# Kernel tuning notes

Hardware: AMD Instinct MI355X
Metric: run time of the kernel (lower is better)

The kernel has to match this reference:

```python
import jax, jax.numpy as jnp
import numpy as np
from jax import lax

DN = ('NCHW', 'OIHW', 'NCHW')


def setup_inputs() -> dict:
    key = jax.random.key(0)
    ks = jax.random.split(key, 7)
    B, IC, OC, H, W = 8, 64, 64, 128, 128
    return {
        'x': jax.random.normal(ks[0], (B, IC, H, W), jnp.float32),
        'w3': jax.random.normal(ks[1], (OC, IC, 3, 3), jnp.float32) * 0.05,
        'b3': jax.random.normal(ks[2], (OC,), jnp.float32) * 0.05,
        'w5': jax.random.normal(ks[3], (OC, IC, 5, 5), jnp.float32) * 0.05,
        'b5': jax.random.normal(ks[4], (OC,), jnp.float32) * 0.05,
        'wr': jax.random.normal(ks[5], (OC, 10, 1, 1), jnp.float32) * 0.1,
        'br': jax.random.normal(ks[6], (OC,), jnp.float32) * 0.05,
    }


def reference(x, w3, b3, w5, b5, wr, br):
    # Two 'same' convs (k=3 pad 1, k=5 pad 2) as in layers['5']
    y3 = lax.conv_general_dilated(x, w3, (1, 1), 'SAME', dimension_numbers=DN) + b3[None, :, None, None]
    y5 = lax.conv_general_dilated(x, w5, (1, 1), 'SAME', dimension_numbers=DN) + b5[None, :, None, None]
    B, C, H, W = y3.shape
    # The nested pad/crop loop == 9 zero-padded unit shifts of y3:
    # stackedFeatures order per channel: [y5, shift(sh=0,sw=0..2), shift(sh=1,...), ...]
    # shifted[h, w] = y3[h + 1 - sw, w + 1 - sh] with zero padding.
    P = jnp.pad(y3, ((0, 0), (0, 0), (1, 1), (1, 1)))
    shifts = [P[:, :, 2 - sw:2 - sw + H, 2 - sh:2 - sh + W]
              for sh in range(3) for sw in range(3)]
    stacked = jnp.stack([y5] + shifts, axis=2)  # [B, C, 10, H, W]
    # remap: grouped 1x1 conv, groups=OC, 10 in-channels per group
    out = jnp.einsum('bcghw,cg->bchw', stacked, wr[:, :, 0, 0]) + br[None, :, None, None]
    return out
```

## Files before the change

### kernel.cpp

```cpp
#include <hip/hip_runtime.h>

typedef unsigned short u16;
typedef unsigned int u32;
typedef __attribute__((ext_vector_type(8))) short short8;
typedef __attribute__((ext_vector_type(4))) short short4v;
typedef __attribute__((ext_vector_type(4))) float floatx4;

#define XP 72

__device__ __forceinline__ float bf2f(u16 u) {
    u32 b = ((u32)u) << 16;
    return __builtin_bit_cast(float, b);
}
__device__ __forceinline__ u16 f2bf(float f) {
    u32 b = __builtin_bit_cast(u32, f);
    b += 0x7FFFu + ((b >> 16) & 1u);
    return (u16)(b >> 16);
}

typedef __attribute__((address_space(3))) u16 lds_u16;
typedef const __attribute__((address_space(1))) u16 glob_u16;
__device__ __forceinline__ void gl_lds16(const u16* g, u16* l) {
    __builtin_amdgcn_global_load_lds((glob_u16*)g, (lds_u16*)l, 16, 0, 0);
}

__device__ __forceinline__ float load_any(const void* p, int i, int isf32) {
    return isf32 ? ((const float*)p)[i] : bf2f(((const u16*)p)[i]);
}

__device__ __forceinline__ int sniff_f(const void* x) {
    u16 u = ((const u16*)x)[2 * (int)threadIdx.x];
    int e = (u >> 7) & 0xFF;
    unsigned long long m = __ballot(e >= 140);
    return __popcll(m) >= 2 ? 1 : 0;
}

#define W5C_BYTE 0
#define SCAL_BYTE 204800
#define V_BYTE 207616
#define FR_BYTE 1272576
#define XT_BYTE 2321152
#define N_W5C 102400
#define N_SCAL 704
#define PACK_N2 (N_W5C + N_SCAL)

#define PACK_BLKS ((PACK_N2 + 255) / 256)
#define TRANS_BLKS 4096

__global__ __launch_bounds__(256) void pack_trans(
        const void* __restrict__ x, const void* __restrict__ w3,
        const void* __restrict__ b3, const void* __restrict__ w5,
        const void* __restrict__ b5, const void* __restrict__ wr,
        const void* __restrict__ br,
        u16* __restrict__ w5c, float* __restrict__ scal,
        u16* __restrict__ xt) {
    __shared__ u16 tbuf[32 * XP];
    const int bid = blockIdx.x;
    const int tid = threadIdx.x;
    const int f = sniff_f(x);

    if (bid < PACK_BLKS) {
        const int i = bid * 256 + tid;
        if (i >= PACK_N2) return;
        if (i < N_W5C) {
            int j = i & 7, lane = (i >> 3) & 63, mt = (i >> 9) & 3, ks = i >> 11;
            int oc = mt * 16 + (lane & 15);
            int k = ks * 32 + ((lane >> 4) & 3) * 8 + j;
            int tap = k >> 6, ic = k & 63;
            int kh = tap / 5, kw = tap - kh * 5;
            int dh = kh - 2, dw = kw - 2;
            float v = load_any(wr, oc * 10, f) * load_any(w5, (oc * 64 + ic) * 25 + tap, f);
            for (int sw = 0; sw < 3; ++sw) {
                int r = dh + sw;
                if (r < 0 || r > 2) continue;
                for (int sh = 0; sh < 3; ++sh) {
                    int c = dw + sh;
                    if (c < 0 || c > 2) continue;
                    v += load_any(wr, oc * 10 + 1 + sh * 3 + sw, f) *
                         load_any(w3, (oc * 64 + ic) * 9 + r * 3 + c, f);
                }
            }
            w5c[i] = f2bf(v);
        } else {
            int i2 = i - N_W5C;
            float v;
            if (i2 < 64) {
                int oc = i2;
                float swr = 0.f;
                for (int g = 1; g <= 9; ++g) swr += load_any(wr, oc * 10 + g, f);
                v = load_any(wr, oc * 10, f) * load_any(b5, oc, f) +
                    swr * load_any(b3, oc, f) + load_any(br, oc, f);
            } else {
                v = load_any(wr, i2 - 64, f);
            }
            scal[i2] = v;
        }
        return;
    }

    {
        const int t2 = bid - PACK_BLKS;
        const int b = t2 >> 9, h = (t2 >> 2) & 127, w0 = (t2 & 3) * 32;
        const int t = tid;
        if (f) {
            const int w2 = t & 15, ic = t >> 4;
#pragma unroll
            for (int p = 0; p < 4; ++p) {
                int icc = ic + p * 16;
                const float* src = (const float*)x +
                    (((size_t)(b * 64 + icc) * 128 + h) * 128 + w0 + 2 * w2);
                float2 v = *(const float2*)src;
                tbuf[(2 * w2) * XP + icc]     = f2bf(v.x);
                tbuf[(2 * w2 + 1) * XP + icc] = f2bf(v.y);
            }
        } else {
            const int w4 = t & 7, ic = t >> 3;
#pragma unroll
            for (int p = 0; p < 2; ++p) {
                int icc = ic + p * 32;
                const u16* src = (const u16*)x +
                    (((size_t)(b * 64 + icc) * 128 + h) * 128 + w0 + 4 * w4);
                short4v v = *(const short4v*)src;
#pragma unroll
                for (int e = 0; e < 4; ++e)
                    tbuf[(4 * w4 + e) * XP + icc] = (u16)v[e];
            }
        }
        __syncthreads();
        const int w = t >> 3, qq = t & 7;
        short8 v = *(const short8*)&tbuf[w * XP + qq * 8];
        *(short8*)(xt + ((size_t)((b * 128 + h) * 128) + w0 + w) * 64 + qq * 8) = v;
    }
}

__global__ __launch_bounds__(256) void virt_y3_mfma(
        const void* __restrict__ x,
        const u16* __restrict__ xt, const void* __restrict__ w3,
        const void* __restrict__ b3, float* __restrict__ V) {
    __shared__ __align__(16) u16 xrow[132 * XP];
    const int side = blockIdx.x, b = blockIdx.y;
    const int tid = threadIdx.x;
    const int f = sniff_f(x);
    const int fixed = (side & 1) ? 127 : 0;
    {
        const int q8 = tid & 7, p0 = tid >> 3;
#pragma unroll
        for (int it = 0; it < 5; ++it) {
            int p = p0 + it * 32;
            if (p < 132) {
                int cc = p - 2;
                short8 v = {0, 0, 0, 0, 0, 0, 0, 0};
                if ((unsigned)cc < 128u) {
                    size_t idx = (side < 2)
                        ? ((size_t)(b * 128 + fixed) * 128 + cc)
                        : ((size_t)(b * 128 + cc) * 128 + fixed);
                    v = *(const short8*)(xt + idx * 64 + q8 * 8);
                }
                *(short8*)&xrow[p * XP + q8 * 8] = v;
            }
        }
    }
    const int wv = tid >> 6, lane = tid & 63, cb = lane & 15, q = lane >> 4;
    const int oc = wv * 16 + cb;
    short8 aaA[6];
#pragma unroll
    for (int ks = 0; ks < 6; ++ks) {
        const int kbase = ks * 32 + q * 8;
        const int kk = kbase >> 6, ic0 = kbase & 63;
        int r, c;
        if (side == 0)      { r = 2;  c = kk; }
        else if (side == 1) { r = 0;  c = kk; }
        else if (side == 2) { r = kk; c = 2;  }
        else                { r = kk; c = 0;  }
        short8 a;
#pragma unroll
        for (int j = 0; j < 8; ++j)
            a[j] = (short)f2bf(load_any(w3, (oc * 64 + ic0 + j) * 9 + r * 3 + c, f));
        aaA[ks] = a;
    }
    __syncthreads();

    floatx4 acc[9];
#pragma unroll
    for (int nt = 0; nt < 9; ++nt) acc[nt] = (floatx4){0.f, 0.f, 0.f, 0.f};
#pragma unroll
    for (int ks = 0; ks < 6; ++ks) {
        const int kbase = ks * 32 + q * 8;
        const int kk = kbase >> 6, ic0 = kbase & 63;
#pragma unroll
        for (int nt = 0; nt < 9; ++nt) {
            int p = nt * 16 + cb + kk;
            if (nt == 8 && p > 131) p = 131;
            short8 bb = *(const short8*)&xrow[p * XP + ic0];
            acc[nt] = __builtin_amdgcn_mfma_f32_16x16x32_bf16(aaA[ks], bb,
                                                              acc[nt], 0, 0, 0);
        }
    }
#pragma unroll
    for (int nt = 0; nt < 9; ++nt) {
        int pos = nt * 16 + cb;
        if (pos < 130) {
#pragma unroll
            for (int reg = 0; reg < 4; ++reg) {
                int oco = wv * 16 + q * 4 + reg;
                V[((size_t)(b * 4 + side) * 130 + pos) * 64 + oco] =
                    acc[nt][reg] + load_any(b3, oco, f);
            }
        }
    }
}

__global__ __launch_bounds__(256) void ring_fix(
        const float* __restrict__ V, const float* __restrict__ scal,
        float* __restrict__ Fr) {
    const int side = blockIdx.x, b = blockIdx.y;
    const float* wrf = scal + 64;
    const float* Vb = V + (size_t)b * 4 * 130 * 64;
    for (int k = 0; k < 8; ++k) {
        const int idx = (blockIdx.z * 8 + k) * 256 + threadIdx.x;
        const int pos = idx >> 6, oc = idx & 63;
        int h, w;
        if (side == 0)      { h = 0;   w = pos; }
        else if (side == 1) { h = 127; w = pos; }
        else if (side == 2) { w = 0;   h = pos; }
        else                { w = 127; h = pos; }
        float s = 0.f;
#pragma unroll
        for (int sh = 0; sh < 3; ++sh)
#pragma unroll
            for (int sw = 0; sw < 3; ++sw) {
                const int qh = h + 1 - sw, qw = w + 1 - sh;
                int sd, pp;
                if (qh == -1)       { sd = 0; pp = qw + 1; }
                else if (qh == 128) { sd = 1; pp = qw + 1; }
                else if (qw == -1)  { sd = 2; pp = qh + 1; }
                else if (qw == 128) { sd = 3; pp = qh + 1; }
                else continue;
                s -= wrf[oc * 10 + 1 + sh * 3 + sw] *
                     Vb[((size_t)sd * 130 + pp) * 64 + oc];
            }
        Fr[((size_t)(b * 4 + side) * 128 + pos) * 64 + oc] = s;
    }
}

__global__ __launch_bounds__(256, 3) void conv_main(
        const void* __restrict__ x,
        const u16* __restrict__ xt, const u16* __restrict__ w5c,
        const float* __restrict__ scal, const float* __restrict__ Fr,
        void* __restrict__ out) {
    __shared__ __align__(16) u16 xs[240 * XP];
    __shared__ __align__(16) u16 wbuf[2][2][2048];
    const int b = blockIdx.z, h0 = blockIdx.y * 8, w0 = blockIdx.x * 16;
    const int tid = threadIdx.x;
    const int wv = tid >> 6, lane = tid & 63;
    const int f = sniff_f(x);

    {
        const int q8 = tid & 7, p0 = tid >> 3;
#pragma unroll
        for (int it = 0; it < 8; ++it) {
            int px = p0 + it * 32;
            if (px < 240) {
                int r = px / 20, c = px - r * 20;
                int gh = h0 + r - 2, gw = w0 + c - 2;
                short8 v = {0, 0, 0, 0, 0, 0, 0, 0};
                if ((unsigned)gh < 128u && (unsigned)gw < 128u)
                    v = *(const short8*)(xt +
                            ((size_t)((b * 128 + gh) * 128 + gw)) * 64 + q8 * 8);
                *(short8*)&xs[px * XP + q8 * 8] = v;
            }
        }
    }
    gl_lds16(w5c + 0 * 2048 + wv * 512 + lane * 8, &wbuf[0][0][wv * 512]);
    gl_lds16(w5c + 1 * 2048 + wv * 512 + lane * 8, &wbuf[0][1][wv * 512]);
    __syncthreads();

    const int cb = lane & 15, q = lane >> 4, wv2 = wv * 2;
    floatx4 acc[4][2];
#pragma unroll
    for (int mt = 0; mt < 4; ++mt)
#pragma unroll
        for (int nt = 0; nt < 2; ++nt)
            acc[mt][nt] = (floatx4){0.f, 0.f, 0.f, 0.f};

#pragma unroll 1
    for (int tap = 0; tap < 25; ++tap) {
        const int p = tap & 1;
        if (tap + 1 < 25) {
            gl_lds16(w5c + (size_t)((tap + 1) * 2 + 0) * 2048 + wv * 512 + lane * 8,
                     &wbuf[p ^ 1][0][wv * 512]);
            gl_lds16(w5c + (size_t)((tap + 1) * 2 + 1) * 2048 + wv * 512 + lane * 8,
                     &wbuf[p ^ 1][1][wv * 512]);
        }
        const int kh = tap / 5, kw = tap - kh * 5;
#pragma unroll
        for (int s = 0; s < 2; ++s) {
            short8 aa[4], bb[2];
#pragma unroll
            for (int mt = 0; mt < 4; ++mt)
                aa[mt] = *(const short8*)&wbuf[p][s][mt * 512 + lane * 8];
#pragma unroll
            for (int nt = 0; nt < 2; ++nt)
                bb[nt] = *(const short8*)&xs[((wv2 + nt + kh) * 20 + cb + kw) * XP +
                                             s * 32 + q * 8];
#pragma unroll
            for (int nt = 0; nt < 2; ++nt)
#pragma unroll
                for (int mt = 0; mt < 4; ++mt)
                    acc[mt][nt] = __builtin_amdgcn_mfma_f32_16x16x32_bf16(
                        aa[mt], bb[nt], acc[mt][nt], 0, 0, 0);
        }
        __syncthreads();
    }

    const float* biasC = scal;
    const float* Frb = Fr + (size_t)b * 4 * 128 * 64;
#pragma unroll
    for (int mt = 0; mt < 4; ++mt)
#pragma unroll
        for (int nt = 0; nt < 2; ++nt) {
            const int gh = h0 + wv2 + nt;
            const int gw = w0 + cb;
            const int oc0 = mt * 16 + q * 4;
            floatx4 s;
#pragma unroll
            for (int reg = 0; reg < 4; ++reg)
                s[reg] = acc[mt][nt][reg] + biasC[oc0 + reg];
            {
                int sd = -1, pp = 0;
                if (gh == 0)        { sd = 0; pp = gw; }
                else if (gh == 127) { sd = 1; pp = gw; }
                else if (gw == 0)   { sd = 2; pp = gh; }
                else if (gw == 127) { sd = 3; pp = gh; }
                if (sd >= 0) {
                    floatx4 fv = *(const floatx4*)(Frb +
                        ((size_t)sd * 128 + pp) * 64 + oc0);
#pragma unroll
                    for (int reg = 0; reg < 4; ++reg) s[reg] += fv[reg];
                }
            }
#pragma unroll
            for (int reg = 0; reg < 4; ++reg) {
                size_t oidx = ((size_t)(b * 64 + oc0 + reg) * 128 + gh) * 128 + gw;
                if (f) ((float*)out)[oidx] = s[reg];
                else   ((u16*)out)[oidx]   = f2bf(s[reg]);
            }
        }
}

extern "C" void kernel_launch(void* const* d_in, const int* in_sizes, int n_in,
                              void* d_out, int out_size, void* d_ws, size_t ws_size,
                              hipStream_t stream) {
    const void* x  = d_in[0];
    const void* w3 = d_in[1];
    const void* b3 = d_in[2];
    const void* w5 = d_in[3];
    const void* b5 = d_in[4];
    const void* wr = d_in[5];
    const void* br = d_in[6];

    u16*   w5c  = (u16*)((char*)d_ws + W5C_BYTE);
    float* scal = (float*)((char*)d_ws + SCAL_BYTE);
    float* V    = (float*)((char*)d_ws + V_BYTE);
    float* Fr   = (float*)((char*)d_ws + FR_BYTE);
    u16*   xt   = (u16*)((char*)d_ws + XT_BYTE);

    pack_trans<<<PACK_BLKS + TRANS_BLKS, 256, 0, stream>>>(
        x, w3, b3, w5, b5, wr, br, w5c, scal, xt);
    virt_y3_mfma<<<dim3(4, 8), 256, 0, stream>>>(x, xt, w3, b3, V);
    ring_fix<<<dim3(4, 8, 4), 256, 0, stream>>>(V, scal, Fr);
    conv_main<<<dim3(8, 16, 8), 256, 0, stream>>>(x, xt, w5c, scal, Fr, d_out);
}
```

Baseline: 167.5 us.

## Double conv_main tile height and stream weights through registers instead of LDS

conv_main's tile grows from 8 to 16 rows, giving 4 rows per wave and a 4x4 MFMA accumulator, so each weight fragment is reused across twice as many output rows. The LDS double-buffered weight staging via global_load_lds and the per-tap __syncthreads are dropped. Each lane now loads its weight fragments straight from global into registers with a two-stage ping-pong (wA/wB) that overlaps with the MFMAs. This adds register pressure (launch_bounds occupancy hint removed), a larger 400-pixel input halo in LDS, and half as many blocks.

Result: faster. 159.0 us (-5.1%).

```diff
diff --git a/kernel.cpp b/kernel.cpp
--- a/kernel.cpp
+++ b/kernel.cpp
@@ -16,12 +16,6 @@
     u32 b = __builtin_bit_cast(u32, f);
     b += 0x7FFFu + ((b >> 16) & 1u);
     return (u16)(b >> 16);
-}
-
-typedef __attribute__((address_space(3))) u16 lds_u16;
-typedef const __attribute__((address_space(1))) u16 glob_u16;
-__device__ __forceinline__ void gl_lds16(const u16* g, u16* l) {
-    __builtin_amdgcn_global_load_lds((glob_u16*)g, (lds_u16*)l, 16, 0, 0);
 }
 
 __device__ __forceinline__ float load_any(const void* p, int i, int isf32) {
@@ -243,24 +237,51 @@
     }
 }
 
-__global__ __launch_bounds__(256, 3) void conv_main(
+#define LOADW(dst, tap)                                                       \
+    {                                                                         \
+        _Pragma("unroll")                                                     \
+        for (int s_ = 0; s_ < 2; ++s_)                                        \
+            _Pragma("unroll")                                                 \
+            for (int mt_ = 0; mt_ < 4; ++mt_)                                 \
+                dst[s_ * 4 + mt_] = *(const short8*)(wp +                     \
+                    (size_t)(tap) * 4096 + s_ * 2048 + mt_ * 512);            \
+    }
+
+#define COMPW(src, tap)                                                       \
+    {                                                                         \
+        const int kh_ = (tap) / 5, kw_ = (tap) - kh_ * 5;                     \
+        _Pragma("unroll")                                                     \
+        for (int s_ = 0; s_ < 2; ++s_) {                                      \
+            short8 bb_[4];                                                    \
+            _Pragma("unroll")                                                 \
+            for (int nt_ = 0; nt_ < 4; ++nt_)                                 \
+                bb_[nt_] = *(const short8*)&xs[((wv4 + nt_ + kh_) * 20 +      \
+                    cb + kw_) * XP + s_ * 32 + q * 8];                        \
+            _Pragma("unroll")                                                 \
+            for (int nt_ = 0; nt_ < 4; ++nt_)                                 \
+                _Pragma("unroll")                                             \
+                for (int mt_ = 0; mt_ < 4; ++mt_)                             \
+                    acc[mt_][nt_] = __builtin_amdgcn_mfma_f32_16x16x32_bf16(  \
+                        src[s_ * 4 + mt_], bb_[nt_], acc[mt_][nt_], 0, 0, 0); \
+        }                                                                     \
+    }
+
+__global__ __launch_bounds__(256) void conv_main(
         const void* __restrict__ x,
         const u16* __restrict__ xt, const u16* __restrict__ w5c,
         const float* __restrict__ scal, const float* __restrict__ Fr,
         void* __restrict__ out) {
-    __shared__ __align__(16) u16 xs[240 * XP];
-    __shared__ __align__(16) u16 wbuf[2][2][2048];
-    const int b = blockIdx.z, h0 = blockIdx.y * 8, w0 = blockIdx.x * 16;
+    __shared__ __align__(16) u16 xs[400 * XP];
+    const int b = blockIdx.z, h0 = blockIdx.y * 16, w0 = blockIdx.x * 16;
     const int tid = threadIdx.x;
     const int wv = tid >> 6, lane = tid & 63;
     const int f = sniff_f(x);
 
     {
         const int q8 = tid & 7, p0 = tid >> 3;
-#pragma unroll
-        for (int it = 0; it < 8; ++it) {
+        for (int it = 0; it < 13; ++it) {
             int px = p0 + it * 32;
-            if (px < 240) {
+            if (px < 400) {
                 int r = px / 20, c = px - r * 20;
                 int gh = h0 + r - 2, gw = w0 + c - 2;
                 short8 v = {0, 0, 0, 0, 0, 0, 0, 0};
@@ -271,55 +292,36 @@
             }
         }
     }
-    gl_lds16(w5c + 0 * 2048 + wv * 512 + lane * 8, &wbuf[0][0][wv * 512]);
-    gl_lds16(w5c + 1 * 2048 + wv * 512 + lane * 8, &wbuf[0][1][wv * 512]);
     __syncthreads();
 
-    const int cb = lane & 15, q = lane >> 4, wv2 = wv * 2;
-    floatx4 acc[4][2];
+    const int cb = lane & 15, q = lane >> 4, wv4 = wv * 4;
+    const u16* wp = w5c + lane * 8;
+    floatx4 acc[4][4];
 #pragma unroll
     for (int mt = 0; mt < 4; ++mt)
 #pragma unroll
-        for (int nt = 0; nt < 2; ++nt)
+        for (int nt = 0; nt < 4; ++nt)
             acc[mt][nt] = (floatx4){0.f, 0.f, 0.f, 0.f};
 
+    short8 wA[8], wB[8];
+    LOADW(wA, 0);
 #pragma unroll 1
-    for (int tap = 0; tap < 25; ++tap) {
-        const int p = tap & 1;
-        if (tap + 1 < 25) {
-            gl_lds16(w5c + (size_t)((tap + 1) * 2 + 0) * 2048 + wv * 512 + lane * 8,
-                     &wbuf[p ^ 1][0][wv * 512]);
-            gl_lds16(w5c + (size_t)((tap + 1) * 2 + 1) * 2048 + wv * 512 + lane * 8,
-                     &wbuf[p ^ 1][1][wv * 512]);
-        }
-        const int kh = tap / 5, kw = tap - kh * 5;
-#pragma unroll
-        for (int s = 0; s < 2; ++s) {
-            short8 aa[4], bb[2];
-#pragma unroll
-            for (int mt = 0; mt < 4; ++mt)
-                aa[mt] = *(const short8*)&wbuf[p][s][mt * 512 + lane * 8];
-#pragma unroll
-            for (int nt = 0; nt < 2; ++nt)
-                bb[nt] = *(const short8*)&xs[((wv2 + nt + kh) * 20 + cb + kw) * XP +
-                                             s * 32 + q * 8];
-#pragma unroll
-            for (int nt = 0; nt < 2; ++nt)
-#pragma unroll
-                for (int mt = 0; mt < 4; ++mt)
-                    acc[mt][nt] = __builtin_amdgcn_mfma_f32_16x16x32_bf16(
-                        aa[mt], bb[nt], acc[mt][nt], 0, 0, 0);
-        }
-        __syncthreads();
-    }
+    for (int t2 = 0; t2 < 12; ++t2) {
+        const int tap = 2 * t2;
+        LOADW(wB, tap + 1);
+        COMPW(wA, tap);
+        LOADW(wA, tap + 2);
+        COMPW(wB, tap + 1);
+    }
+    COMPW(wA, 24);
 
     const float* biasC = scal;
     const float* Frb = Fr + (size_t)b * 4 * 128 * 64;
 #pragma unroll
     for (int mt = 0; mt < 4; ++mt)
 #pragma unroll
-        for (int nt = 0; nt < 2; ++nt) {
-            const int gh = h0 + wv2 + nt;
+        for (int nt = 0; nt < 4; ++nt) {
+            const int gh = h0 + wv4 + nt;
             const int gw = w0 + cb;
             const int oc0 = mt * 16 + q * 4;
             floatx4 s;
@@ -369,5 +371,5 @@
         x, w3, b3, w5, b5, wr, br, w5c, scal, xt);
     virt_y3_mfma<<<dim3(4, 8), 256, 0, stream>>>(x, xt, w3, b3, V);
     ring_fix<<<dim3(4, 8, 4), 256, 0, stream>>>(V, scal, Fr);
-    conv_main<<<dim3(8, 16, 8), 256, 0, stream>>>(x, xt, w5c, scal, Fr, d_out);
-}
+    conv_main<<<dim3(8, 8, 8), 256, 0, stream>>>(x, xt, w5c, scal, Fr, d_out);
+}
```
